# Kernel optimization log

Hardware: AMD Instinct MI355X
Metric: run time of the kernel (lower is better)

## Reference

```python
import jax, jax.numpy as jnp
import numpy as np

DA = 256      # aux input feature dim
DENSE = 512   # SLAM dense units


def setup_inputs() -> dict:
    key = jax.random.key(0)
    k1, k2, k3, k4 = jax.random.split(key, 4)
    x_main = jax.random.normal(k1, (1, 128, 512, 256), dtype=jnp.float32)  # [1,T,M,K]
    x_aux = jax.random.normal(k2, (256, 128, DA), dtype=jnp.float32)       # [K,T,Da]
    W = jax.random.normal(k3, (DA, DENSE), dtype=jnp.float32) / np.sqrt(DA)
    b = jax.random.normal(k4, (DENSE,), dtype=jnp.float32) * 0.01
    return {"x_main": x_main, "x_aux": x_aux, "W": W, "b": b}


def reference(x_main, x_aux, W, b):
    # SLAM aux dense (+relu), applied to every aux slice at once: [K,T,Da] -> [K,T,dense]
    aux_out = jax.nn.relu(jnp.einsum("ktd,de->kte", x_aux, W) + b)
    main = jnp.squeeze(x_main, axis=0)  # [T,M,K]
    # per-slice matmul main[t] @ aux_out[:,t,:] batched over T
    stacked = jnp.einsum("tmk,kte->tme", main, aux_out)  # [T,M,dense]
    # expand_dims(-1) then expand_dims(0)
    return stacked[None, :, :, :, None]  # [1,T,M,dense,1]
```

## Files before the change

### kernel.cpp

```cpp
#include <hip/hip_runtime.h>


typedef __attribute__((ext_vector_type(8))) short  bf16x8;
typedef __attribute__((ext_vector_type(4))) float  f32x4;
typedef __attribute__((ext_vector_type(4))) unsigned int uint4v;
typedef __attribute__((ext_vector_type(2))) unsigned int uint2v;

#define T_DIM 128
#define M_DIM 512
#define K_DIM 256
#define DA    256
#define DENSE 512
#define CHUNK_T_STRIDE 131072
#define CHUNK_G_STRIDE 4096

__device__ __forceinline__ unsigned short f2bf(float f) {
    unsigned u = __builtin_bit_cast(unsigned, f);
    unsigned r = (u + 0x7fffu + ((u >> 16) & 1u)) >> 16;
    return (unsigned short)r;
}
__device__ __forceinline__ unsigned pack2(float lo, float hi) {
    return (unsigned)f2bf(lo) | ((unsigned)f2bf(hi) << 16);
}

__global__ __launch_bounds__(256) void wchunk_kernel(const float* __restrict__ W,
                                                     unsigned short* __restrict__ Wc) {
    int c = blockIdx.x * 256 + threadIdx.x;
    int g = c >> 9;
    int e = c & 511;
    float f[8];
#pragma unroll
    for (int j = 0; j < 8; ++j) f[j] = W[(g * 8 + j) * DENSE + e];
    uint4v w;
    w.x = pack2(f[0], f[1]); w.y = pack2(f[2], f[3]);
    w.z = pack2(f[4], f[5]); w.w = pack2(f[6], f[7]);
    *reinterpret_cast<uint4v*>(Wc + (size_t)c * 8) = w;
}

__global__ __launch_bounds__(256) void aux_kernel(const float* __restrict__ xaux,
                                                  const unsigned short* __restrict__ Wc,
                                                  const float* __restrict__ bias,
                                                  unsigned short* __restrict__ auxc) {
    __shared__ unsigned short xa[64 * 264];
    const int bid = blockIdx.x;
    const int swz = (bid & 7) * 128 + (bid >> 3);
    const int t  = swz >> 3;
    const int r  = swz & 7;
    const int kb = (r >> 1) * 64;
    const int eb = (r & 1) * 256;
    const int tid = threadIdx.x, lane = tid & 63, wid = tid >> 6;
    const int l15 = lane & 15, lg = lane >> 4;
    char* xab = reinterpret_cast<char*>(xa);

#pragma unroll
    for (int j = 0; j < 16; ++j) {
        int kr = wid + 4 * j;
        const float* src = xaux + ((size_t)(kb + kr) * T_DIM + t) * DA + lane * 4;
        f32x4 v = *reinterpret_cast<const f32x4*>(src);
        uint2v o; o.x = pack2(v.x, v.y); o.y = pack2(v.z, v.w);
        *reinterpret_cast<uint2v*>(xab + kr * 528 + lane * 8) = o;
    }
    __syncthreads();

    const int we = wid * 64;
    f32x4 acc[4][4];
#pragma unroll
    for (int i = 0; i < 4; ++i)
#pragma unroll
        for (int j = 0; j < 4; ++j) acc[i][j] = (f32x4)0.0f;

#define AUX_LOAD_WF(dst, dsv)                                                              \
    do {                                                                                   \
        _Pragma("unroll") for (int j = 0; j < 4; ++j) {                                    \
            int e = eb + we + j * 16 + l15;                                                \
            dst[j] = *reinterpret_cast<const bf16x8*>(                                     \
                Wc + (size_t)((dsv) * 4 + lg) * CHUNK_G_STRIDE + (size_t)e * 8);           \
        }                                                                                  \
    } while (0)

#define AUX_COMPUTE(wfc, dsv)                                                              \
    do {                                                                                   \
        bf16x8 xf[4];                                                                      \
        _Pragma("unroll") for (int i = 0; i < 4; ++i)                                      \
            xf[i] = *reinterpret_cast<const bf16x8*>(                                      \
                xab + (i * 16 + l15) * 528 + ((dsv) * 4 + lg) * 16);                       \
        _Pragma("unroll") for (int i = 0; i < 4; ++i)                                      \
            _Pragma("unroll") for (int j = 0; j < 4; ++j)                                  \
                acc[i][j] = __builtin_amdgcn_mfma_f32_16x16x32_bf16(xf[i], wfc[j], acc[i][j], 0, 0, 0); \
    } while (0)

    bf16x8 wfA[4], wfB[4];
    AUX_LOAD_WF(wfA, 0);
#pragma unroll
    for (int ds = 0; ds < 8; ds += 2) {
        AUX_LOAD_WF(wfB, ds + 1);
        AUX_COMPUTE(wfA, ds);
        if (ds + 2 < 8) { AUX_LOAD_WF(wfA, ds + 2); }
        AUX_COMPUTE(wfB, ds + 1);
    }
#undef AUX_LOAD_WF
#undef AUX_COMPUTE

#pragma unroll
    for (int i = 0; i < 4; ++i) {
        int k0 = kb + i * 16 + lg * 4;
#pragma unroll
        for (int j = 0; j < 4; ++j) {
            int e = eb + we + j * 16 + l15;
            float bv = bias[e];
            float v0 = fmaxf(acc[i][j].x + bv, 0.0f);
            float v1 = fmaxf(acc[i][j].y + bv, 0.0f);
            float v2 = fmaxf(acc[i][j].z + bv, 0.0f);
            float v3 = fmaxf(acc[i][j].w + bv, 0.0f);
            uint2 o; o.x = pack2(v0, v1); o.y = pack2(v2, v3);
            size_t idx = (size_t)t * CHUNK_T_STRIDE + (size_t)(k0 >> 3) * CHUNK_G_STRIDE
                       + (size_t)e * 8 + (k0 & 7);
            *reinterpret_cast<uint2*>(auxc + idx) = o;
        }
    }
}

#define MS_STRIDE 72
#define MS_BUF    (128 * MS_STRIDE)
__global__ __launch_bounds__(256) void main_kernel(const float* __restrict__ xmain,
                                                   const unsigned short* __restrict__ auxc,
                                                   float* __restrict__ out) {
    __shared__ char ms[2 * MS_BUF];
    const int bid = blockIdx.x;
    const int swz = ((bid & 7) << 8) | (bid >> 3);
    const int t   = swz >> 4;
    const int r4  = swz & 15;
    const int eb  = (r4 & 3) * 128;
    const int mb  = (r4 >> 2) * 128;
    const int tid  = threadIdx.x;
    const int lane = tid & 63, wid = tid >> 6;
    const int wm = (wid & 1) * 64;
    const int we = (wid >> 1) * 64;
    const int l15 = lane & 15, lg = lane >> 4;

    const float* At = xmain + (size_t)t * M_DIM * K_DIM;
    const unsigned short* Ct = auxc + (size_t)t * CHUNK_T_STRIDE;

    const int srow = tid >> 3;
    const int skof = tid & 7;

    f32x4 acc[4][4];
#pragma unroll
    for (int i = 0; i < 4; ++i)
#pragma unroll
        for (int j = 0; j < 4; ++j) acc[i][j] = (f32x4)0.0f;

#define MS_LOAD(regs, ksv)                                                                 \
    do {                                                                                   \
        _Pragma("unroll") for (int p = 0; p < 4; ++p)                                      \
            regs[p] = *reinterpret_cast<const f32x4*>(                                     \
                At + (size_t)(mb + p * 32 + srow) * K_DIM + (ksv) * 32 + skof * 4);        \
    } while (0)

#define MS_WRITE(regs, bufv)                                                               \
    do {                                                                                   \
        _Pragma("unroll") for (int p = 0; p < 4; ++p) {                                    \
            uint2v o;                                                                      \
            o.x = pack2(regs[p].x, regs[p].y);                                             \
            o.y = pack2(regs[p].z, regs[p].w);                                             \
            *reinterpret_cast<uint2v*>(ms + (bufv) * MS_BUF                                \
                                          + (p * 32 + srow) * MS_STRIDE + skof * 8) = o;   \
        }                                                                                  \
    } while (0)

    f32x4 sreg[4];
    MS_LOAD(sreg, 0);
    MS_WRITE(sreg, 0);
    __syncthreads();

#pragma unroll
    for (int ks = 0; ks < 8; ++ks) {
        const int cur = ks & 1;
        if (ks < 7) MS_LOAD(sreg, ks + 1);

        bf16x8 af[4], mf[4];
#pragma unroll
        for (int i = 0; i < 4; ++i)
            af[i] = *reinterpret_cast<const bf16x8*>(
                Ct + (size_t)(ks * 4 + lg) * CHUNK_G_STRIDE
                   + (size_t)(eb + we + i * 16 + l15) * 8);
#pragma unroll
        for (int j = 0; j < 4; ++j)
            mf[j] = *reinterpret_cast<const bf16x8*>(
                ms + cur * MS_BUF + (wm + j * 16 + l15) * MS_STRIDE + lg * 16);
#pragma unroll
        for (int i = 0; i < 4; ++i)
#pragma unroll
            for (int j = 0; j < 4; ++j)
                acc[i][j] = __builtin_amdgcn_mfma_f32_16x16x32_bf16(af[i], mf[j], acc[i][j], 0, 0, 0);

        if (ks < 7) {
            MS_WRITE(sreg, cur ^ 1);
            __syncthreads();
        }
    }
#undef MS_LOAD
#undef MS_WRITE

#pragma unroll
    for (int i = 0; i < 4; ++i) {
        int e0 = eb + we + i * 16 + lg * 4;
#pragma unroll
        for (int j = 0; j < 4; ++j) {
            int m = mb + wm + j * 16 + l15;
            *reinterpret_cast<f32x4*>(out + (size_t)t * M_DIM * DENSE + (size_t)m * DENSE + e0) = acc[i][j];
        }
    }
}

extern "C" void kernel_launch(void* const* d_in, const int* in_sizes, int n_in,
                              void* d_out, int out_size, void* d_ws, size_t ws_size,
                              hipStream_t stream) {
    const float* x_main = (const float*)d_in[0];
    const float* x_aux  = (const float*)d_in[1];
    const float* W      = (const float*)d_in[2];
    const float* b      = (const float*)d_in[3];
    float* out = (float*)d_out;

    unsigned short* Wc   = (unsigned short*)d_ws;
    unsigned short* auxc = (unsigned short*)((char*)d_ws + (1u << 19));

    wchunk_kernel<<<64, 256, 0, stream>>>(W, Wc);
    aux_kernel<<<1024, 256, 0, stream>>>(x_aux, Wc, b, auxc);
    main_kernel<<<2048, 256, 0, stream>>>(x_main, auxc, out);
}
```

Measured before the change: 269.3 us.

## Fuse aux dense+relu into main matmul via LDS-resident intermediate

Merges the aux projection and the per-slice batched matmul into one kernel. Each 1024-thread block computes relu(x_aux·W+b) for one t and a 64-wide dense slice into LDS, then multiplies x_main[t] by it. This removes the global bf16 intermediate write and re-read and one kernel launch. In exchange, blocks re-read x_main and x_aux more often across dense slices, and large LDS use limits occupancy.

```diff
diff --git a/kernel.cpp b/kernel.cpp
--- a/kernel.cpp
+++ b/kernel.cpp
@@ -11,8 +11,7 @@
 #define K_DIM 256
 #define DA    256
 #define DENSE 512
-#define CHUNK_T_STRIDE 131072
-#define CHUNK_G_STRIDE 4096
+#define WC_G_STRIDE 4096
 
 __device__ __forceinline__ unsigned short f2bf(float f) {
     unsigned u = __builtin_bit_cast(unsigned, f);
@@ -37,124 +36,108 @@
     *reinterpret_cast<uint4v*>(Wc + (size_t)c * 8) = w;
 }
 
-__global__ __launch_bounds__(256) void aux_kernel(const float* __restrict__ xaux,
-                                                  const unsigned short* __restrict__ Wc,
-                                                  const float* __restrict__ bias,
-                                                  unsigned short* __restrict__ auxc) {
-    __shared__ unsigned short xa[64 * 264];
+__global__ __launch_bounds__(1024, 4) void fused_kernel(const float* __restrict__ xmain,
+                                                        const float* __restrict__ xaux,
+                                                        const unsigned short* __restrict__ Wc,
+                                                        const float* __restrict__ bias,
+                                                        float* __restrict__ out) {
+    __shared__ char lds[98304];
+    char* const auxl = lds + 65536;
+
     const int bid = blockIdx.x;
     const int swz = (bid & 7) * 128 + (bid >> 3);
-    const int t  = swz >> 3;
-    const int r  = swz & 7;
-    const int kb = (r >> 1) * 64;
-    const int eb = (r & 1) * 256;
-    const int tid = threadIdx.x, lane = tid & 63, wid = tid >> 6;
-    const int l15 = lane & 15, lg = lane >> 4;
-    char* xab = reinterpret_cast<char*>(xa);
-
-#pragma unroll
-    for (int j = 0; j < 16; ++j) {
-        int kr = wid + 4 * j;
-        const float* src = xaux + ((size_t)(kb + kr) * T_DIM + t) * DA + lane * 4;
-        f32x4 v = *reinterpret_cast<const f32x4*>(src);
-        uint2v o; o.x = pack2(v.x, v.y); o.y = pack2(v.z, v.w);
-        *reinterpret_cast<uint2v*>(xab + kr * 528 + lane * 8) = o;
-    }
-    __syncthreads();
-
-    const int we = wid * 64;
-    f32x4 acc[4][4];
-#pragma unroll
-    for (int i = 0; i < 4; ++i)
-#pragma unroll
-        for (int j = 0; j < 4; ++j) acc[i][j] = (f32x4)0.0f;
-
-#define AUX_LOAD_WF(dst, dsv)                                                              \
-    do {                                                                                   \
-        _Pragma("unroll") for (int j = 0; j < 4; ++j) {                                    \
-            int e = eb + we + j * 16 + l15;                                                \
-            dst[j] = *reinterpret_cast<const bf16x8*>(                                     \
-                Wc + (size_t)((dsv) * 4 + lg) * CHUNK_G_STRIDE + (size_t)e * 8);           \
-        }                                                                                  \
-    } while (0)
-
-#define AUX_COMPUTE(wfc, dsv)                                                              \
-    do {                                                                                   \
-        bf16x8 xf[4];                                                                      \
-        _Pragma("unroll") for (int i = 0; i < 4; ++i)                                      \
-            xf[i] = *reinterpret_cast<const bf16x8*>(                                      \
-                xab + (i * 16 + l15) * 528 + ((dsv) * 4 + lg) * 16);                       \
-        _Pragma("unroll") for (int i = 0; i < 4; ++i)                                      \
-            _Pragma("unroll") for (int j = 0; j < 4; ++j)                                  \
-                acc[i][j] = __builtin_amdgcn_mfma_f32_16x16x32_bf16(xf[i], wfc[j], acc[i][j], 0, 0, 0); \
-    } while (0)
-
-    bf16x8 wfA[4], wfB[4];
-    AUX_LOAD_WF(wfA, 0);
-#pragma unroll
-    for (int ds = 0; ds < 8; ds += 2) {
-        AUX_LOAD_WF(wfB, ds + 1);
-        AUX_COMPUTE(wfA, ds);
-        if (ds + 2 < 8) { AUX_LOAD_WF(wfA, ds + 2); }
-        AUX_COMPUTE(wfB, ds + 1);
-    }
-#undef AUX_LOAD_WF
-#undef AUX_COMPUTE
-
-#pragma unroll
-    for (int i = 0; i < 4; ++i) {
-        int k0 = kb + i * 16 + lg * 4;
-#pragma unroll
-        for (int j = 0; j < 4; ++j) {
-            int e = eb + we + j * 16 + l15;
-            float bv = bias[e];
-            float v0 = fmaxf(acc[i][j].x + bv, 0.0f);
-            float v1 = fmaxf(acc[i][j].y + bv, 0.0f);
-            float v2 = fmaxf(acc[i][j].z + bv, 0.0f);
-            float v3 = fmaxf(acc[i][j].w + bv, 0.0f);
-            uint2 o; o.x = pack2(v0, v1); o.y = pack2(v2, v3);
-            size_t idx = (size_t)t * CHUNK_T_STRIDE + (size_t)(k0 >> 3) * CHUNK_G_STRIDE
-                       + (size_t)e * 8 + (k0 & 7);
-            *reinterpret_cast<uint2*>(auxc + idx) = o;
-        }
-    }
-}
-
-#define MS_STRIDE 72
-#define MS_BUF    (128 * MS_STRIDE)
-__global__ __launch_bounds__(256) void main_kernel(const float* __restrict__ xmain,
-                                                   const unsigned short* __restrict__ auxc,
-                                                   float* __restrict__ out) {
-    __shared__ char ms[2 * MS_BUF];
-    const int bid = blockIdx.x;
-    const int swz = ((bid & 7) << 8) | (bid >> 3);
-    const int t   = swz >> 4;
-    const int r4  = swz & 15;
-    const int eb  = (r4 & 3) * 128;
-    const int mb  = (r4 >> 2) * 128;
+    const int t   = swz >> 3;
+    const int eb  = (swz & 7) * 64;
+
     const int tid  = threadIdx.x;
     const int lane = tid & 63, wid = tid >> 6;
-    const int wm = (wid & 1) * 64;
-    const int we = (wid >> 1) * 64;
-    const int l15 = lane & 15, lg = lane >> 4;
-
-    const float* At = xmain + (size_t)t * M_DIM * K_DIM;
-    const unsigned short* Ct = auxc + (size_t)t * CHUNK_T_STRIDE;
-
+    const int l15  = lane & 15, lg = lane >> 4;
     const int srow = tid >> 3;
-    const int skof = tid & 7;
-
-    f32x4 acc[4][4];
-#pragma unroll
-    for (int i = 0; i < 4; ++i)
-#pragma unroll
-        for (int j = 0; j < 4; ++j) acc[i][j] = (f32x4)0.0f;
+    const int sq   = tid & 7;
+
+    const int wk = (wid >> 2) * 64;
+    const int we = (wid & 3) * 16;
+    const float bias_v = bias[eb + we + l15];
+
+    f32x4 acc1[4];
+#pragma unroll
+    for (int i = 0; i < 4; ++i) acc1[i] = (f32x4)0.0f;
+
+#define XA_LOAD(regs, dsv)                                                                 \
+    do {                                                                                   \
+        _Pragma("unroll") for (int p = 0; p < 2; ++p)                                      \
+            regs[p] = *reinterpret_cast<const f32x4*>(                                     \
+                xaux + (size_t)(p * 128 + srow) * (T_DIM * DA) + (size_t)t * DA            \
+                     + (dsv) * 32 + sq * 4);                                               \
+    } while (0)
+
+#define XA_WRITE(regs, bufv)                                                               \
+    do {                                                                                   \
+        _Pragma("unroll") for (int p = 0; p < 2; ++p) {                                    \
+            uint2v o;                                                                      \
+            o.x = pack2(regs[p].x, regs[p].y);                                             \
+            o.y = pack2(regs[p].z, regs[p].w);                                             \
+            *reinterpret_cast<uint2v*>(lds + (bufv) * 16384 + (sq >> 1) * 4096             \
+                                          + (p * 128 + srow) * 16 + (sq & 1) * 8) = o;     \
+        }                                                                                  \
+    } while (0)
+
+#define WF_LOAD(dst, dsv)                                                                  \
+    dst = *reinterpret_cast<const bf16x8*>(                                                \
+        Wc + (size_t)((dsv) * 4 + lg) * WC_G_STRIDE + (size_t)(eb + we + l15) * 8)
+
+    {
+        f32x4 s1[2];
+        bf16x8 wfA, wfB;
+        XA_LOAD(s1, 0);
+        WF_LOAD(wfA, 0);
+        XA_WRITE(s1, 0);
+        __syncthreads();
+#pragma unroll
+        for (int ds = 0; ds < 8; ++ds) {
+            const int cur = ds & 1;
+            if (ds < 7) { XA_LOAD(s1, ds + 1); WF_LOAD(wfB, ds + 1); }
+            bf16x8 xf[4];
+#pragma unroll
+            for (int i = 0; i < 4; ++i)
+                xf[i] = *reinterpret_cast<const bf16x8*>(
+                    lds + cur * 16384 + lg * 4096 + (wk + i * 16 + l15) * 16);
+#pragma unroll
+            for (int i = 0; i < 4; ++i)
+                acc1[i] = __builtin_amdgcn_mfma_f32_16x16x32_bf16(xf[i], wfA, acc1[i], 0, 0, 0);
+            if (ds < 7) { XA_WRITE(s1, cur ^ 1); __syncthreads(); wfA = wfB; }
+        }
+    }
+#undef XA_LOAD
+#undef XA_WRITE
+#undef WF_LOAD
+
+#pragma unroll
+    for (int i = 0; i < 4; ++i) {
+        int k0 = wk + i * 16 + lg * 4;
+        float v0 = fmaxf(acc1[i].x + bias_v, 0.0f);
+        float v1 = fmaxf(acc1[i].y + bias_v, 0.0f);
+        float v2 = fmaxf(acc1[i].z + bias_v, 0.0f);
+        float v3 = fmaxf(acc1[i].w + bias_v, 0.0f);
+        uint2v o; o.x = pack2(v0, v1); o.y = pack2(v2, v3);
+        *reinterpret_cast<uint2v*>(auxl + (k0 >> 3) * 1024 + (we + l15) * 16 + (k0 & 7) * 2) = o;
+    }
+
+    const int wm  = (wid >> 1) * 64;
+    const int we2 = (wid & 1) * 32;
+
+    f32x4 acc2[2][4];
+#pragma unroll
+    for (int i = 0; i < 2; ++i)
+#pragma unroll
+        for (int j = 0; j < 4; ++j) acc2[i][j] = (f32x4)0.0f;
 
 #define MS_LOAD(regs, ksv)                                                                 \
     do {                                                                                   \
         _Pragma("unroll") for (int p = 0; p < 4; ++p)                                      \
             regs[p] = *reinterpret_cast<const f32x4*>(                                     \
-                At + (size_t)(mb + p * 32 + srow) * K_DIM + (ksv) * 32 + skof * 4);        \
+                xmain + (size_t)t * (M_DIM * K_DIM) + (size_t)(p * 128 + srow) * K_DIM     \
+                      + (ksv) * 32 + sq * 4);                                              \
     } while (0)
 
 #define MS_WRITE(regs, bufv)                                                               \
@@ -163,52 +146,48 @@
             uint2v o;                                                                      \
             o.x = pack2(regs[p].x, regs[p].y);                                             \
             o.y = pack2(regs[p].z, regs[p].w);                                             \
-            *reinterpret_cast<uint2v*>(ms + (bufv) * MS_BUF                                \
-                                          + (p * 32 + srow) * MS_STRIDE + skof * 8) = o;   \
+            *reinterpret_cast<uint2v*>(lds + (bufv) * 32768 + (sq >> 1) * 8192             \
+                                          + (p * 128 + srow) * 16 + (sq & 1) * 8) = o;     \
         }                                                                                  \
     } while (0)
 
-    f32x4 sreg[4];
-    MS_LOAD(sreg, 0);
-    MS_WRITE(sreg, 0);
-    __syncthreads();
-
-#pragma unroll
-    for (int ks = 0; ks < 8; ++ks) {
-        const int cur = ks & 1;
-        if (ks < 7) MS_LOAD(sreg, ks + 1);
-
-        bf16x8 af[4], mf[4];
-#pragma unroll
-        for (int i = 0; i < 4; ++i)
-            af[i] = *reinterpret_cast<const bf16x8*>(
-                Ct + (size_t)(ks * 4 + lg) * CHUNK_G_STRIDE
-                   + (size_t)(eb + we + i * 16 + l15) * 8);
-#pragma unroll
-        for (int j = 0; j < 4; ++j)
-            mf[j] = *reinterpret_cast<const bf16x8*>(
-                ms + cur * MS_BUF + (wm + j * 16 + l15) * MS_STRIDE + lg * 16);
-#pragma unroll
-        for (int i = 0; i < 4; ++i)
+    {
+        f32x4 s2[4];
+        MS_LOAD(s2, 0);
+        __syncthreads();
+        MS_WRITE(s2, 0);
+        __syncthreads();
+#pragma unroll
+        for (int ks = 0; ks < 8; ++ks) {
+            const int cur = ks & 1;
+            if (ks < 7) MS_LOAD(s2, ks + 1);
+            bf16x8 af[2], mf[4];
+#pragma unroll
+            for (int i = 0; i < 2; ++i)
+                af[i] = *reinterpret_cast<const bf16x8*>(
+                    auxl + (ks * 4 + lg) * 1024 + (we2 + i * 16 + l15) * 16);
 #pragma unroll
             for (int j = 0; j < 4; ++j)
-                acc[i][j] = __builtin_amdgcn_mfma_f32_16x16x32_bf16(af[i], mf[j], acc[i][j], 0, 0, 0);
-
-        if (ks < 7) {
-            MS_WRITE(sreg, cur ^ 1);
-            __syncthreads();
+                mf[j] = *reinterpret_cast<const bf16x8*>(
+                    lds + cur * 32768 + lg * 8192 + (wm + j * 16 + l15) * 16);
+#pragma unroll
+            for (int i = 0; i < 2; ++i)
+#pragma unroll
+                for (int j = 0; j < 4; ++j)
+                    acc2[i][j] = __builtin_amdgcn_mfma_f32_16x16x32_bf16(af[i], mf[j], acc2[i][j], 0, 0, 0);
+            if (ks < 7) { MS_WRITE(s2, cur ^ 1); __syncthreads(); }
         }
     }
 #undef MS_LOAD
 #undef MS_WRITE
 
 #pragma unroll
-    for (int i = 0; i < 4; ++i) {
-        int e0 = eb + we + i * 16 + lg * 4;
+    for (int i = 0; i < 2; ++i) {
+        int e0 = eb + we2 + i * 16 + lg * 4;
 #pragma unroll
         for (int j = 0; j < 4; ++j) {
-            int m = mb + wm + j * 16 + l15;
-            *reinterpret_cast<f32x4*>(out + (size_t)t * M_DIM * DENSE + (size_t)m * DENSE + e0) = acc[i][j];
+            int m = wm + j * 16 + l15;
+            *reinterpret_cast<f32x4*>(out + (size_t)t * (M_DIM * DENSE) + (size_t)m * DENSE + e0) = acc2[i][j];
         }
     }
 }
@@ -222,10 +201,8 @@
     const float* b      = (const float*)d_in[3];
     float* out = (float*)d_out;
 
-    unsigned short* Wc   = (unsigned short*)d_ws;
-    unsigned short* auxc = (unsigned short*)((char*)d_ws + (1u << 19));
+    unsigned short* Wc = (unsigned short*)d_ws;
 
     wchunk_kernel<<<64, 256, 0, stream>>>(W, Wc);
-    aux_kernel<<<1024, 256, 0, stream>>>(x_aux, Wc, b, auxc);
-    main_kernel<<<2048, 256, 0, stream>>>(x_main, auxc, out);
-}
+    fused_kernel<<<1024, 1024, 0, stream>>>(x_main, x_aux, Wc, b, out);
+}
```

Measured after the change: 290.8 us. 8.0% more time.

## Stage main-input tiles per wave in swizzled LDS and prefetch aux fragments

Applied to the files above, without the earlier changes.

Each wave now converts and stages its own 64-row slice of the fp32 main input into a private, XOR-swizzled LDS region. This removes every block-wide __syncthreads from the K loop. Aux fragments are software-pipelined into double-buffered registers one K step ahead, and the launch bounds now request 3 blocks per CU. The cost is that waves sharing the same M rows each load them from global memory, which doubles x_main traffic seen by L2. Register pressure also rises.

```diff
diff --git a/kernel.cpp b/kernel.cpp
--- a/kernel.cpp
+++ b/kernel.cpp
@@ -120,87 +120,91 @@
     }
 }
 
-#define MS_STRIDE 72
-#define MS_BUF    (128 * MS_STRIDE)
-__global__ __launch_bounds__(256) void main_kernel(const float* __restrict__ xmain,
-                                                   const unsigned short* __restrict__ auxc,
-                                                   float* __restrict__ out) {
-    __shared__ char ms[2 * MS_BUF];
+__global__ __launch_bounds__(256, 3) void main_kernel(const float* __restrict__ xmain,
+                                                      const unsigned short* __restrict__ auxc,
+                                                      float* __restrict__ out) {
+    __shared__ char mlds[32768];
     const int bid = blockIdx.x;
     const int swz = ((bid & 7) << 8) | (bid >> 3);
     const int t   = swz >> 4;
     const int r4  = swz & 15;
     const int eb  = (r4 & 3) * 128;
     const int mb  = (r4 >> 2) * 128;
-    const int tid  = threadIdx.x;
-    const int lane = tid & 63, wid = tid >> 6;
+    const int lane = threadIdx.x & 63, wid = threadIdx.x >> 6;
     const int wm = (wid & 1) * 64;
     const int we = (wid >> 1) * 64;
     const int l15 = lane & 15, lg = lane >> 4;
-
-    const float* At = xmain + (size_t)t * M_DIM * K_DIM;
+    const int sr = lane >> 3;
+    const int sk = lane & 7;
+    const int sg = sk >> 1, sh = sk & 1;
+
+    char* const wbase = mlds + wid * 8192;
+    const float* Atw = xmain + (size_t)t * (M_DIM * K_DIM) + (size_t)(mb + wm) * K_DIM;
     const unsigned short* Ct = auxc + (size_t)t * CHUNK_T_STRIDE;
 
-    const int srow = tid >> 3;
-    const int skof = tid & 7;
-
     f32x4 acc[4][4];
 #pragma unroll
     for (int i = 0; i < 4; ++i)
 #pragma unroll
         for (int j = 0; j < 4; ++j) acc[i][j] = (f32x4)0.0f;
 
-#define MS_LOAD(regs, ksv)                                                                 \
-    do {                                                                                   \
-        _Pragma("unroll") for (int p = 0; p < 4; ++p)                                      \
-            regs[p] = *reinterpret_cast<const f32x4*>(                                     \
-                At + (size_t)(mb + p * 32 + srow) * K_DIM + (ksv) * 32 + skof * 4);        \
-    } while (0)
-
-#define MS_WRITE(regs, bufv)                                                               \
-    do {                                                                                   \
-        _Pragma("unroll") for (int p = 0; p < 4; ++p) {                                    \
+    f32x4  ms[8];
+    bf16x8 afr[2][4];
+
+#define MF_GLOAD(ksv)                                                                      \
+    do {                                                                                   \
+        _Pragma("unroll") for (int q = 0; q < 8; ++q)                                      \
+            ms[q] = *reinterpret_cast<const f32x4*>(                                       \
+                Atw + (size_t)(q * 8 + sr) * K_DIM + (ksv) * 32 + sk * 4);                 \
+    } while (0)
+
+#define MF_WRITE(bufv)                                                                    \
+    do {                                                                                   \
+        _Pragma("unroll") for (int q = 0; q < 8; ++q) {                                    \
             uint2v o;                                                                      \
-            o.x = pack2(regs[p].x, regs[p].y);                                             \
-            o.y = pack2(regs[p].z, regs[p].w);                                             \
-            *reinterpret_cast<uint2v*>(ms + (bufv) * MS_BUF                                \
-                                          + (p * 32 + srow) * MS_STRIDE + skof * 8) = o;   \
+            o.x = pack2(ms[q].x, ms[q].y);                                                 \
+            o.y = pack2(ms[q].z, ms[q].w);                                                 \
+            int byte = sg * 1024 + (q * 8 + sr) * 16 + sh * 8;                             \
+            byte ^= (sg << 4);                                                             \
+            *reinterpret_cast<uint2v*>(wbase + (bufv) * 4096 + byte) = o;                  \
         }                                                                                  \
     } while (0)
 
-    f32x4 sreg[4];
-    MS_LOAD(sreg, 0);
-    MS_WRITE(sreg, 0);
-    __syncthreads();
+#define AF_GLOAD(slot, ksv)                                                                \
+    do {                                                                                   \
+        _Pragma("unroll") for (int i = 0; i < 4; ++i)                                      \
+            afr[slot][i] = *reinterpret_cast<const bf16x8*>(                               \
+                Ct + (size_t)((ksv) * 4 + lg) * CHUNK_G_STRIDE                             \
+                   + (size_t)(eb + we + i * 16 + l15) * 8);                                \
+    } while (0)
+
+    MF_GLOAD(0);
+    AF_GLOAD(0, 0);
+    MF_WRITE(0);
 
 #pragma unroll
     for (int ks = 0; ks < 8; ++ks) {
         const int cur = ks & 1;
-        if (ks < 7) MS_LOAD(sreg, ks + 1);
-
-        bf16x8 af[4], mf[4];
+        if (ks < 7) { MF_GLOAD(ks + 1); AF_GLOAD(cur ^ 1, ks + 1); }
+
+        bf16x8 mf[4];
+#pragma unroll
+        for (int j = 0; j < 4; ++j) {
+            int byte = lg * 1024 + (j * 16 + l15) * 16;
+            byte ^= (lg << 4);
+            mf[j] = *reinterpret_cast<const bf16x8*>(wbase + cur * 4096 + byte);
+        }
 #pragma unroll
         for (int i = 0; i < 4; ++i)
-            af[i] = *reinterpret_cast<const bf16x8*>(
-                Ct + (size_t)(ks * 4 + lg) * CHUNK_G_STRIDE
-                   + (size_t)(eb + we + i * 16 + l15) * 8);
-#pragma unroll
-        for (int j = 0; j < 4; ++j)
-            mf[j] = *reinterpret_cast<const bf16x8*>(
-                ms + cur * MS_BUF + (wm + j * 16 + l15) * MS_STRIDE + lg * 16);
-#pragma unroll
-        for (int i = 0; i < 4; ++i)
 #pragma unroll
             for (int j = 0; j < 4; ++j)
-                acc[i][j] = __builtin_amdgcn_mfma_f32_16x16x32_bf16(af[i], mf[j], acc[i][j], 0, 0, 0);
-
-        if (ks < 7) {
-            MS_WRITE(sreg, cur ^ 1);
-            __syncthreads();
-        }
-    }
-#undef MS_LOAD
-#undef MS_WRITE
+                acc[i][j] = __builtin_amdgcn_mfma_f32_16x16x32_bf16(afr[cur][i], mf[j], acc[i][j], 0, 0, 0);
+
+        if (ks < 7) MF_WRITE(cur ^ 1);
+    }
+#undef MF_GLOAD
+#undef MF_WRITE
+#undef AF_GLOAD
 
 #pragma unroll
     for (int i = 0; i < 4; ++i) {
@@ -208,7 +212,7 @@
 #pragma unroll
         for (int j = 0; j < 4; ++j) {
             int m = mb + wm + j * 16 + l15;
-            *reinterpret_cast<f32x4*>(out + (size_t)t * M_DIM * DENSE + (size_t)m * DENSE + e0) = acc[i][j];
+            *reinterpret_cast<f32x4*>(out + (size_t)t * (M_DIM * DENSE) + (size_t)m * DENSE + e0) = acc[i][j];
         }
     }
 }
```

After: 309.2 us. 1.15x slower.
